# Kernel optimization log

Hardware: AMD Instinct MI355X
Metric: run time of the kernel (lower is better)

## Reference

```python
import jax, jax.numpy as jnp
import numpy as np

WH, WW = 8, 8
NUM_HEADS = 12
DIM = 384
N = WH * WW

def _rel_pos_index():
    # Swin relative position index, static [N, N] int array
    coords = np.stack(np.meshgrid(np.arange(WH), np.arange(WW), indexing='ij'))  # [2, wh, ww]
    cf = coords.reshape(2, -1)                      # [2, N]
    rel = cf[:, :, None] - cf[:, None, :]           # [2, N, N]
    rel = rel.transpose(1, 2, 0).copy()             # [N, N, 2]
    rel[..., 0] += WH - 1
    rel[..., 1] += WW - 1
    rel[..., 0] *= 2 * WW - 1
    return jnp.asarray(rel.sum(-1))                 # [N, N]

REL_IDX = _rel_pos_index()


def setup_inputs() -> dict:
    key = jax.random.key(0)
    ks = jax.random.split(key, 4)
    Bn = 4096
    x = jax.random.normal(ks[0], (Bn, N, DIM), dtype=jnp.float32)
    qkv_w = jax.random.normal(ks[1], (3 * DIM, DIM), dtype=jnp.float32) * 0.02
    qkv_b = jnp.zeros((3 * DIM,), dtype=jnp.float32)
    proj_w = jax.random.normal(ks[2], (DIM, DIM), dtype=jnp.float32) * 0.02
    proj_b = jnp.zeros((DIM,), dtype=jnp.float32)
    bias_table = jax.random.normal(ks[3], ((2 * WH - 1) * (2 * WW - 1), NUM_HEADS), dtype=jnp.float32) * 0.02
    return {"x": x, "qkv_w": qkv_w, "qkv_b": qkv_b, "proj_w": proj_w, "proj_b": proj_b, "bias_table": bias_table}


def reference(x, qkv_w, qkv_b, proj_w, proj_b, bias_table):
    Bn, n, C = x.shape
    H = NUM_HEADS
    hd = C // H
    scale = hd ** (-0.5)
    qkv = (x @ qkv_w.T + qkv_b).reshape(Bn, n, 3, H, hd)
    q = qkv[:, :, 0].transpose(0, 2, 1, 3)  # [Bn, H, n, hd]
    k = qkv[:, :, 1].transpose(0, 2, 1, 3)
    v = qkv[:, :, 2].transpose(0, 2, 1, 3)
    attn = jnp.einsum('bhqd,bhkd->bhqk', q, k) * scale  # [Bn, H, n, n]
    bias = bias_table[REL_IDX]                           # [n, n, H]
    attn = attn + bias.transpose(2, 0, 1)[None]          # add rel-pos bias
    attn = jax.nn.softmax(attn, axis=-1)
    out = jnp.einsum('bhqk,bhkd->bqhd', attn, v).reshape(Bn, n, C)
    return out @ proj_w.T + proj_b
```

## Files before the change

kernel.cpp:

```cpp
#include <hip/hip_runtime.h>

#define NT 64
#define NH 12
#define HD 32
#define DIM 384
#define NWIN 4096
#define TPB 512
#define PTPB 256
#define PROWS 64

typedef __bf16 bf16;
typedef __bf16 bf16x8 __attribute__((ext_vector_type(8)));
typedef __bf16 bf16x4 __attribute__((ext_vector_type(4)));
typedef float floatx4 __attribute__((ext_vector_type(4)));

__device__ bf16 g_wqkv[3 * DIM * DIM];
__device__ bf16 g_wproj[DIM * DIM];

__global__ void convert_weights(const float* __restrict__ qkv_w,
                                const float* __restrict__ proj_w) {
    int i = blockIdx.x * blockDim.x + threadIdx.x;
    if (i < 3 * DIM * DIM) g_wqkv[i] = (bf16)qkv_w[i];
    if (i < DIM * DIM)     g_wproj[i] = (bf16)proj_w[i];
}

__global__ __launch_bounds__(TPB, 2) void attn_kernel(
    const float* __restrict__ x,
    const float* __restrict__ qkv_b,
    const float* __restrict__ bias_table,
    float* __restrict__ out)
{
    __shared__ __align__(16) char smem[NT * 392 * 2];
    bf16 (*sx)[392]  = (bf16(*)[392])smem;
    bf16 (*sq)[40]   = (bf16(*)[40])(smem);
    bf16 (*sk)[40]   = (bf16(*)[40])(smem + 5120);
    bf16 (*svT)[72]  = (bf16(*)[72])(smem + 10240);
    bf16 (*spb)[72]  = (bf16(*)[72])(smem + 14848);
    float (*sp)[66]  = (float(*)[66])(smem + 24064);

    const int t    = threadIdx.x;
    const int win  = blockIdx.x;
    const int wave = t >> 6;
    const int lane = t & 63;
    const int quad = lane >> 4;
    const int l15  = lane & 15;

    {
        const float4* src = (const float4*)(x + (size_t)win * (NT * DIM));
        #pragma unroll
        for (int it = 0; it < (NT * DIM / 4) / TPB; ++it) {
            int i = t + it * TPB;
            float4 fv = src[i];
            int r = i / (DIM / 4);
            int c = (i % (DIM / 4)) * 4;
            bf16x4 bv;
            bv[0] = (bf16)fv.x; bv[1] = (bf16)fv.y;
            bv[2] = (bf16)fv.z; bv[3] = (bf16)fv.w;
            *(bf16x4*)&sx[r][c] = bv;
        }
    }
    __syncthreads();

    const int mt   = wave & 3;
    const int half = wave >> 2;
    bf16x8 afrag[DIM / 32];
    #pragma unroll
    for (int ks = 0; ks < DIM / 32; ++ks)
        afrag[ks] = *(const bf16x8*)&sx[mt * 16 + l15][ks * 32 + quad * 8];
    __syncthreads();

    const float scale = 0.17677669529663687f;
    float* outw = out + (size_t)win * (NT * DIM);

    #pragma unroll 1
    for (int h = 0; h < NH; ++h) {
        #pragma unroll
        for (int jj = 0; jj < 3; ++jj) {
            int nt = half * 3 + jj;
            int s  = nt >> 1;
            int nh = (nt & 1) * 16;
            int wrow = s * DIM + h * HD + nh + l15;
            const bf16* Wp = g_wqkv + (size_t)wrow * DIM + quad * 8;
            floatx4 acc = {0.f, 0.f, 0.f, 0.f};
            #pragma unroll
            for (int ks = 0; ks < DIM / 32; ++ks) {
                bf16x8 b = *(const bf16x8*)(Wp + ks * 32);
                acc = __builtin_amdgcn_mfma_f32_16x16x32_bf16(afrag[ks], b, acc, 0, 0, 0);
            }
            float bv = qkv_b[wrow];
            #pragma unroll
            for (int r = 0; r < 4; ++r) {
                int m = mt * 16 + quad * 4 + r;
                float v = acc[r] + bv;
                if (s == 0)      sq[m][nh + l15] = (bf16)(v * scale);
                else if (s == 1) sk[m][nh + l15] = (bf16)v;
                else             svT[nh + l15][m] = (bf16)v;
            }
        }
        __syncthreads();

        #pragma unroll
        for (int jj = 0; jj < 2; ++jj) {
            int job = wave + jj * 8;
            int it = job & 3, jt = job >> 2;
            bf16x8 a = *(const bf16x8*)&sq[it * 16 + l15][quad * 8];
            bf16x8 b = *(const bf16x8*)&sk[jt * 16 + l15][quad * 8];
            floatx4 acc = {0.f, 0.f, 0.f, 0.f};
            acc = __builtin_amdgcn_mfma_f32_16x16x32_bf16(a, b, acc, 0, 0, 0);
            #pragma unroll
            for (int r = 0; r < 4; ++r) {
                int i = it * 16 + quad * 4 + r;
                int j = jt * 16 + l15;
                int yi = i >> 3, xi = i & 7, yj = j >> 3, xj = j & 7;
                int idx = (yi - yj + 7) * 15 + (xi - xj + 7);
                sp[i][j] = acc[r] + bias_table[idx * NH + h];
            }
        }
        __syncthreads();

        {
            int r = t >> 3;
            int o = (t & 7) * 8;
            float e[8];
            float mx = -1e30f;
            #pragma unroll
            for (int c = 0; c < 8; ++c) { e[c] = sp[r][o + c]; mx = fmaxf(mx, e[c]); }
            mx = fmaxf(mx, __shfl_xor(mx, 1));
            mx = fmaxf(mx, __shfl_xor(mx, 2));
            mx = fmaxf(mx, __shfl_xor(mx, 4));
            float sum = 0.f;
            #pragma unroll
            for (int c = 0; c < 8; ++c) { e[c] = __expf(e[c] - mx); sum += e[c]; }
            sum += __shfl_xor(sum, 1);
            sum += __shfl_xor(sum, 2);
            sum += __shfl_xor(sum, 4);
            float inv = 1.0f / sum;
            bf16x8 pv;
            #pragma unroll
            for (int c = 0; c < 8; ++c) pv[c] = (bf16)(e[c] * inv);
            *(bf16x8*)&spb[r][o] = pv;
        }
        __syncthreads();

        {
            int pmt = wave & 3, pnt = wave >> 2;
            floatx4 acc = {0.f, 0.f, 0.f, 0.f};
            #pragma unroll
            for (int ks = 0; ks < 2; ++ks) {
                bf16x8 a = *(const bf16x8*)&spb[pmt * 16 + l15][ks * 32 + quad * 8];
                bf16x8 b = *(const bf16x8*)&svT[pnt * 16 + l15][ks * 32 + quad * 8];
                acc = __builtin_amdgcn_mfma_f32_16x16x32_bf16(a, b, acc, 0, 0, 0);
            }
            #pragma unroll
            for (int r = 0; r < 4; ++r) {
                int m = pmt * 16 + quad * 4 + r;
                outw[(size_t)m * DIM + h * HD + pnt * 16 + l15] = acc[r];
            }
        }
        __syncthreads();
    }
}

__global__ __launch_bounds__(PTPB, 2) void proj_kernel(
    const float* __restrict__ proj_b,
    float* __restrict__ out)
{
    __shared__ __align__(16) bf16 sa[PROWS][392];
    const int t    = threadIdx.x;
    const int wave = t >> 6;
    const int lane = t & 63;
    const int quad = lane >> 4;
    const int l15  = lane & 15;
    float* base = out + (size_t)blockIdx.x * (PROWS * DIM);

    {
        const float4* src = (const float4*)base;
        #pragma unroll
        for (int it = 0; it < (PROWS * DIM / 4) / PTPB; ++it) {
            int i = t + it * PTPB;
            float4 fv = src[i];
            int r = i / (DIM / 4);
            int c = (i % (DIM / 4)) * 4;
            bf16x4 bv;
            bv[0] = (bf16)fv.x; bv[1] = (bf16)fv.y;
            bv[2] = (bf16)fv.z; bv[3] = (bf16)fv.w;
            *(bf16x4*)&sa[r][c] = bv;
        }
    }
    __syncthreads();

    bf16x8 afrag[DIM / 32];
    #pragma unroll
    for (int ks = 0; ks < DIM / 32; ++ks)
        afrag[ks] = *(const bf16x8*)&sa[wave * 16 + l15][ks * 32 + quad * 8];

    #pragma unroll 1
    for (int nt = 0; nt < DIM / 16; ++nt) {
        const bf16* Wp = g_wproj + (size_t)(nt * 16 + l15) * DIM + quad * 8;
        floatx4 acc = {0.f, 0.f, 0.f, 0.f};
        #pragma unroll
        for (int ks = 0; ks < DIM / 32; ++ks) {
            bf16x8 b = *(const bf16x8*)(Wp + ks * 32);
            acc = __builtin_amdgcn_mfma_f32_16x16x32_bf16(afrag[ks], b, acc, 0, 0, 0);
        }
        float pb = proj_b[nt * 16 + l15];
        #pragma unroll
        for (int r = 0; r < 4; ++r)
            base[(size_t)(wave * 16 + quad * 4 + r) * DIM + nt * 16 + l15] = acc[r] + pb;
    }
}

extern "C" void kernel_launch(void* const* d_in, const int* in_sizes, int n_in,
                              void* d_out, int out_size, void* d_ws, size_t ws_size,
                              hipStream_t stream) {
    const float* x          = (const float*)d_in[0];
    const float* qkv_w      = (const float*)d_in[1];
    const float* qkv_b      = (const float*)d_in[2];
    const float* proj_w     = (const float*)d_in[3];
    const float* proj_b     = (const float*)d_in[4];
    const float* bias_table = (const float*)d_in[5];
    float* out = (float*)d_out;

    convert_weights<<<dim3((3 * DIM * DIM + 255) / 256), dim3(256), 0, stream>>>(qkv_w, proj_w);
    attn_kernel<<<dim3(NWIN), dim3(TPB), 0, stream>>>(x, qkv_b, bias_table, out);
    proj_kernel<<<dim3(NWIN), dim3(PTPB), 0, stream>>>(proj_b, out);
}
```

Before: 2.763 ms.

## Process two heads per iteration with shared-memory bias and batched weight loads

The attention kernel now handles two heads per loop iteration, which halves the number of barriers per window and gives each wave more independent MFMA work. The relative-position bias is transposed once in the weight-conversion kernel and staged per head in shared memory, replacing scattered global gathers. Softmax writes the bf16 probabilities in place over the fp32 scores buffer. Weight fragments are loaded into registers ahead of the MFMA chain in both kernels, and the launch bounds are raised. Shared memory grows to about 64KB, which may limit occupancy and raise register pressure.

```diff
diff --git a/kernel.cpp b/kernel.cpp
--- a/kernel.cpp
+++ b/kernel.cpp
@@ -7,36 +7,40 @@
 #define NWIN 4096
 #define TPB 512
 #define PTPB 256
-#define PROWS 64
 
 typedef __bf16 bf16;
 typedef __bf16 bf16x8 __attribute__((ext_vector_type(8)));
 typedef __bf16 bf16x4 __attribute__((ext_vector_type(4)));
 typedef float floatx4 __attribute__((ext_vector_type(4)));
 
-__device__ bf16 g_wqkv[3 * DIM * DIM];
-__device__ bf16 g_wproj[DIM * DIM];
+__device__ __align__(16) bf16 g_wqkv[3 * DIM * DIM];
+__device__ __align__(16) bf16 g_wproj[DIM * DIM];
+__device__ __align__(16) float g_biasT[NH * 225];
 
 __global__ void convert_weights(const float* __restrict__ qkv_w,
-                                const float* __restrict__ proj_w) {
+                                const float* __restrict__ proj_w,
+                                const float* __restrict__ bias_table) {
     int i = blockIdx.x * blockDim.x + threadIdx.x;
     if (i < 3 * DIM * DIM) g_wqkv[i] = (bf16)qkv_w[i];
     if (i < DIM * DIM)     g_wproj[i] = (bf16)proj_w[i];
-}
-
-__global__ __launch_bounds__(TPB, 2) void attn_kernel(
+    if (i < NH * 225) {
+        int h = i / 225, ix = i % 225;
+        g_biasT[i] = bias_table[ix * NH + h];
+    }
+}
+
+__global__ __launch_bounds__(TPB, 4) void attn_kernel(
     const float* __restrict__ x,
     const float* __restrict__ qkv_b,
-    const float* __restrict__ bias_table,
     float* __restrict__ out)
 {
-    __shared__ __align__(16) char smem[NT * 392 * 2];
-    bf16 (*sx)[392]  = (bf16(*)[392])smem;
-    bf16 (*sq)[40]   = (bf16(*)[40])(smem);
-    bf16 (*sk)[40]   = (bf16(*)[40])(smem + 5120);
-    bf16 (*svT)[72]  = (bf16(*)[72])(smem + 10240);
-    bf16 (*spb)[72]  = (bf16(*)[72])(smem + 14848);
-    float (*sp)[66]  = (float(*)[66])(smem + 24064);
+    __shared__ __align__(16) char smem[65288];
+    bf16 (*sx)[392]      = (bf16(*)[392])smem;
+    bf16 (*sq2)[64][40]  = (bf16(*)[64][40])smem;
+    bf16 (*sk2)[64][40]  = (bf16(*)[64][40])(smem + 10240);
+    bf16 (*svT2)[32][72] = (bf16(*)[32][72])(smem + 20480);
+    float (*sp2)[64][66] = (float(*)[64][66])(smem + 29696);
+    float (*sbias)[225]  = (float(*)[225])(smem + 63488);
 
     const int t    = threadIdx.x;
     const int win  = blockIdx.x;
@@ -61,8 +65,8 @@
     }
     __syncthreads();
 
-    const int mt   = wave & 3;
-    const int half = wave >> 2;
+    const int mt  = wave & 3;
+    const int grp = wave >> 2;
     bf16x8 afrag[DIM / 32];
     #pragma unroll
     for (int ks = 0; ks < DIM / 32; ++ks)
@@ -73,38 +77,47 @@
     float* outw = out + (size_t)win * (NT * DIM);
 
     #pragma unroll 1
-    for (int h = 0; h < NH; ++h) {
-        #pragma unroll
-        for (int jj = 0; jj < 3; ++jj) {
-            int nt = half * 3 + jj;
-            int s  = nt >> 1;
-            int nh = (nt & 1) * 16;
-            int wrow = s * DIM + h * HD + nh + l15;
+    for (int hp = 0; hp < NH / 2; ++hp) {
+        if (t < 225)                      sbias[0][t]       = g_biasT[(hp * 2 + 0) * 225 + t];
+        else if (t >= 256 && t < 481)     sbias[1][t - 256] = g_biasT[(hp * 2 + 1) * 225 + (t - 256)];
+
+        #pragma unroll
+        for (int jj = 0; jj < 6; ++jj) {
+            const int hl  = jj / 3;
+            const int j3  = jj % 3;
+            const int nt  = grp * 3 + j3;
+            const int s   = nt >> 1;
+            const int nhh = (nt & 1) * 16;
+            const int h   = hp * 2 + hl;
+            const int wrow = s * DIM + h * HD + nhh + l15;
             const bf16* Wp = g_wqkv + (size_t)wrow * DIM + quad * 8;
+            bf16x8 b[12];
+            #pragma unroll
+            for (int ks = 0; ks < 12; ++ks) b[ks] = *(const bf16x8*)(Wp + ks * 32);
             floatx4 acc = {0.f, 0.f, 0.f, 0.f};
             #pragma unroll
-            for (int ks = 0; ks < DIM / 32; ++ks) {
-                bf16x8 b = *(const bf16x8*)(Wp + ks * 32);
-                acc = __builtin_amdgcn_mfma_f32_16x16x32_bf16(afrag[ks], b, acc, 0, 0, 0);
-            }
+            for (int ks = 0; ks < 12; ++ks)
+                acc = __builtin_amdgcn_mfma_f32_16x16x32_bf16(afrag[ks], b[ks], acc, 0, 0, 0);
             float bv = qkv_b[wrow];
             #pragma unroll
             for (int r = 0; r < 4; ++r) {
                 int m = mt * 16 + quad * 4 + r;
                 float v = acc[r] + bv;
-                if (s == 0)      sq[m][nh + l15] = (bf16)(v * scale);
-                else if (s == 1) sk[m][nh + l15] = (bf16)v;
-                else             svT[nh + l15][m] = (bf16)v;
-            }
-        }
-        __syncthreads();
-
-        #pragma unroll
-        for (int jj = 0; jj < 2; ++jj) {
+                if (s == 0)      sq2[hl][m][nhh + l15] = (bf16)(v * scale);
+                else if (s == 1) sk2[hl][m][nhh + l15] = (bf16)v;
+                else             svT2[hl][nhh + l15][m] = (bf16)v;
+            }
+        }
+        __syncthreads();
+
+        #pragma unroll
+        for (int jj = 0; jj < 4; ++jj) {
             int job = wave + jj * 8;
-            int it = job & 3, jt = job >> 2;
-            bf16x8 a = *(const bf16x8*)&sq[it * 16 + l15][quad * 8];
-            bf16x8 b = *(const bf16x8*)&sk[jt * 16 + l15][quad * 8];
+            int hl = job >> 4;
+            int j4 = job & 15;
+            int it = j4 & 3, jt = j4 >> 2;
+            bf16x8 a = *(const bf16x8*)&sq2[hl][it * 16 + l15][quad * 8];
+            bf16x8 b = *(const bf16x8*)&sk2[hl][jt * 16 + l15][quad * 8];
             floatx4 acc = {0.f, 0.f, 0.f, 0.f};
             acc = __builtin_amdgcn_mfma_f32_16x16x32_bf16(a, b, acc, 0, 0, 0);
             #pragma unroll
@@ -113,44 +126,63 @@
                 int j = jt * 16 + l15;
                 int yi = i >> 3, xi = i & 7, yj = j >> 3, xj = j & 7;
                 int idx = (yi - yj + 7) * 15 + (xi - xj + 7);
-                sp[i][j] = acc[r] + bias_table[idx * NH + h];
+                sp2[hl][i][j] = acc[r] + sbias[hl][idx];
             }
         }
         __syncthreads();
 
         {
-            int r = t >> 3;
-            int o = (t & 7) * 8;
-            float e[8];
+            int r4 = t >> 2;
+            int hl = r4 >> 6;
+            int r  = r4 & 63;
+            int o  = (t & 3) * 16;
+            const float2* pr = (const float2*)&sp2[hl][r][0];
+            float e[16];
             float mx = -1e30f;
             #pragma unroll
-            for (int c = 0; c < 8; ++c) { e[c] = sp[r][o + c]; mx = fmaxf(mx, e[c]); }
+            for (int c = 0; c < 8; ++c) {
+                float2 f2 = pr[(o >> 1) + c];
+                e[2 * c] = f2.x; e[2 * c + 1] = f2.y;
+                mx = fmaxf(mx, fmaxf(f2.x, f2.y));
+            }
             mx = fmaxf(mx, __shfl_xor(mx, 1));
             mx = fmaxf(mx, __shfl_xor(mx, 2));
-            mx = fmaxf(mx, __shfl_xor(mx, 4));
             float sum = 0.f;
             #pragma unroll
-            for (int c = 0; c < 8; ++c) { e[c] = __expf(e[c] - mx); sum += e[c]; }
+            for (int c = 0; c < 16; ++c) { e[c] = __expf(e[c] - mx); sum += e[c]; }
             sum += __shfl_xor(sum, 1);
             sum += __shfl_xor(sum, 2);
-            sum += __shfl_xor(sum, 4);
             float inv = 1.0f / sum;
-            bf16x8 pv;
-            #pragma unroll
-            for (int c = 0; c < 8; ++c) pv[c] = (bf16)(e[c] * inv);
-            *(bf16x8*)&spb[r][o] = pv;
-        }
-        __syncthreads();
-
-        {
-            int pmt = wave & 3, pnt = wave >> 2;
+            bf16* pw = (bf16*)&sp2[hl][r][0];
+            #pragma unroll
+            for (int k = 0; k < 4; ++k) {
+                bf16x4 pv;
+                #pragma unroll
+                for (int z = 0; z < 4; ++z) pv[z] = (bf16)(e[4 * k + z] * inv);
+                *(bf16x4*)&pw[o + 4 * k] = pv;
+            }
+        }
+        __syncthreads();
+
+        #pragma unroll
+        for (int jj = 0; jj < 2; ++jj) {
+            int job = wave + jj * 8;
+            int hl = job >> 3;
+            int j3 = job & 7;
+            int pmt = j3 & 3, pnt = j3 >> 2;
+            const bf16* prow = (const bf16*)&sp2[hl][pmt * 16 + l15][0];
             floatx4 acc = {0.f, 0.f, 0.f, 0.f};
             #pragma unroll
             for (int ks = 0; ks < 2; ++ks) {
-                bf16x8 a = *(const bf16x8*)&spb[pmt * 16 + l15][ks * 32 + quad * 8];
-                bf16x8 b = *(const bf16x8*)&svT[pnt * 16 + l15][ks * 32 + quad * 8];
-                acc = __builtin_amdgcn_mfma_f32_16x16x32_bf16(a, b, acc, 0, 0, 0);
-            }
+                bf16x4 a0 = *(const bf16x4*)&prow[ks * 32 + quad * 8];
+                bf16x4 a1 = *(const bf16x4*)&prow[ks * 32 + quad * 8 + 4];
+                bf16x8 av;
+                #pragma unroll
+                for (int z = 0; z < 4; ++z) { av[z] = a0[z]; av[z + 4] = a1[z]; }
+                bf16x8 b = *(const bf16x8*)&svT2[hl][pnt * 16 + l15][ks * 32 + quad * 8];
+                acc = __builtin_amdgcn_mfma_f32_16x16x32_bf16(av, b, acc, 0, 0, 0);
+            }
+            int h = hp * 2 + hl;
             #pragma unroll
             for (int r = 0; r < 4; ++r) {
                 int m = pmt * 16 + quad * 4 + r;
@@ -161,22 +193,22 @@
     }
 }
 
-__global__ __launch_bounds__(PTPB, 2) void proj_kernel(
+__global__ __launch_bounds__(PTPB, 3) void proj_kernel(
     const float* __restrict__ proj_b,
     float* __restrict__ out)
 {
-    __shared__ __align__(16) bf16 sa[PROWS][392];
+    __shared__ __align__(16) bf16 sa[NT][392];
     const int t    = threadIdx.x;
     const int wave = t >> 6;
     const int lane = t & 63;
     const int quad = lane >> 4;
     const int l15  = lane & 15;
-    float* base = out + (size_t)blockIdx.x * (PROWS * DIM);
+    float* base = out + (size_t)blockIdx.x * (NT * DIM);
 
     {
         const float4* src = (const float4*)base;
         #pragma unroll
-        for (int it = 0; it < (PROWS * DIM / 4) / PTPB; ++it) {
+        for (int it = 0; it < (NT * DIM / 4) / PTPB; ++it) {
             int i = t + it * PTPB;
             float4 fv = src[i];
             int r = i / (DIM / 4);
@@ -194,15 +226,16 @@
     for (int ks = 0; ks < DIM / 32; ++ks)
         afrag[ks] = *(const bf16x8*)&sa[wave * 16 + l15][ks * 32 + quad * 8];
 
-    #pragma unroll 1
+    #pragma unroll
     for (int nt = 0; nt < DIM / 16; ++nt) {
         const bf16* Wp = g_wproj + (size_t)(nt * 16 + l15) * DIM + quad * 8;
+        bf16x8 b[12];
+        #pragma unroll
+        for (int ks = 0; ks < 12; ++ks) b[ks] = *(const bf16x8*)(Wp + ks * 32);
         floatx4 acc = {0.f, 0.f, 0.f, 0.f};
         #pragma unroll
-        for (int ks = 0; ks < DIM / 32; ++ks) {
-            bf16x8 b = *(const bf16x8*)(Wp + ks * 32);
-            acc = __builtin_amdgcn_mfma_f32_16x16x32_bf16(afrag[ks], b, acc, 0, 0, 0);
-        }
+        for (int ks = 0; ks < 12; ++ks)
+            acc = __builtin_amdgcn_mfma_f32_16x16x32_bf16(afrag[ks], b[ks], acc, 0, 0, 0);
         float pb = proj_b[nt * 16 + l15];
         #pragma unroll
         for (int r = 0; r < 4; ++r)
@@ -221,7 +254,7 @@
     const float* bias_table = (const float*)d_in[5];
     float* out = (float*)d_out;
 
-    convert_weights<<<dim3((3 * DIM * DIM + 255) / 256), dim3(256), 0, stream>>>(qkv_w, proj_w);
-    attn_kernel<<<dim3(NWIN), dim3(TPB), 0, stream>>>(x, qkv_b, bias_table, out);
+    convert_weights<<<dim3((3 * DIM * DIM + 255) / 256), dim3(256), 0, stream>>>(qkv_w, proj_w, bias_table);
+    attn_kernel<<<dim3(NWIN), dim3(TPB), 0, stream>>>(x, qkv_b, out);
     proj_kernel<<<dim3(NWIN), dim3(PTPB), 0, stream>>>(proj_b, out);
 }
```

After: 2.649 ms. 4.1% less time.
